# Kernel optimization log

Hardware: AMD Instinct MI355X
Metric: run time of the kernel (lower is better)

The kernel has to match this reference:

```python
import jax, jax.numpy as jnp
import numpy as np
from jax import lax

B, NM, P, F, E, H, K = 32, 131072, 256, 3, 64, 4, 3
DH = E // H


def layer_norm(x, gamma, beta, eps=1e-5):
    mu = x.mean(-1, keepdims=True)
    var = ((x - mu) ** 2).mean(-1, keepdims=True)
    return (x - mu) * lax.rsqrt(var + eps) * gamma + beta


def knn_interp(x, pos_x, pos_y, k=K):
    """x: [B, Nx, F] features at pos_x [Nx, 2]; interpolate to pos_y [Ny, 2].
    Positions are shared across the batch (they are tiled in the torch code),
    so KNN indices/weights are computed once. Matches torch knn + inverse-
    squared-distance weighted scatter (uniform per-batch counts => gather form).
    """
    d2 = jnp.sum((pos_y[:, None, :] - pos_x[None, :, :]) ** 2, axis=-1)  # [Ny, Nx]
    neg_d2, idx = lax.top_k(-d2, k)                                      # [Ny, k]
    w = 1.0 / jnp.clip(-neg_d2, 1e-16)                                   # [Ny, k]
    w = lax.stop_gradient(w)  # torch computes weights under no_grad
    gathered = x[:, idx, :]                                              # [B, Ny, k, F]
    num = jnp.sum(gathered * w[None, :, :, None], axis=2)                # [B, Ny, F]
    den = jnp.sum(w, axis=1)[None, :, None]                              # [1, Ny, 1]
    return num / den


def setup_inputs() -> dict:
    key = jax.random.key(0)
    ks = jax.random.split(key, 8)
    return {
        "node_attr": jax.random.normal(ks[0], (B * NM, F), jnp.float32),
        "position_mesh": jax.random.uniform(ks[1], (NM, 2), jnp.float32),
        "position_pivotal": jax.random.uniform(ks[2], (P, 2), jnp.float32),
        "ln_gamma": jnp.ones((F,), jnp.float32),
        "ln_beta": jnp.zeros((F,), jnp.float32),
        "Wf": jax.random.normal(ks[3], (E, F), jnp.float32) * (2.0 / E) ** 0.5,
        "bf": jnp.zeros((E,), jnp.float32),
        "Wp": jax.random.normal(ks[4], (E, 2), jnp.float32) * (2.0 / E) ** 0.5,
        "bp": jnp.zeros((E,), jnp.float32),
        "in_proj_w": jax.random.normal(ks[5], (3 * E, E), jnp.float32) * (1.0 / E) ** 0.5,
        "in_proj_b": jnp.zeros((3 * E,), jnp.float32),
        "batch_size": B,
    }


def reference(node_attr, position_mesh, position_pivotal, ln_gamma, ln_beta,
              Wf, bf, Wp, bp, in_proj_w, in_proj_b, batch_size):
    x = node_attr.reshape(batch_size, -1, F)                 # [B, NM, F]
    # PivotalNorm after encoder (encoder/decoder MeshGraphNet omitted: undefined dep)
    x = layer_norm(x, ln_gamma, ln_beta)
    # ---- downsample: mesh -> pivotal via inverse-distance KNN interpolation ----
    y = knn_interp(x, position_mesh, position_pivotal)       # [B, P, F]
    # attention-based pooling over pivotal nodes
    q = (jnp.einsum('bpf,ef->bpe', y, Wf) + bf
         + (position_pivotal @ Wp.T + bp)[None])             # [B, P, E]
    Wq, Wk = in_proj_w[:E], in_proj_w[E:2 * E]
    bq, bk = in_proj_b[:E], in_proj_b[E:2 * E]
    Q = (q @ Wq.T + bq).reshape(batch_size, P, H, DH)
    Kt = (q @ Wk.T + bk).reshape(batch_size, P, H, DH)
    scores = jnp.einsum('bqhd,bkhd->bhqk', Q, Kt) / np.float32(np.sqrt(DH))
    attn = jax.nn.softmax(scores, axis=-1)                   # [B, H, P, P]
    attn_w = attn.mean(axis=1)                               # avg heads, [B, P, P]
    y = jnp.einsum('bqk,bkf->bqf', attn_w, y)                # [B, P, F]
    # ---- interpolate: pivotal -> mesh ----
    out = knn_interp(y, position_pivotal, position_mesh)     # [B, NM, F]
    return out.reshape(-1, F)
```

## Files before the change

### kernel.cpp

```cpp
#include <hip/hip_runtime.h>
#include <math.h>

#define NM 131072
#define PP 256
#define BB 32

#define CHUNKS 512
#define CHUNK_SZ 256

#define INF_F 3.0e38f

__device__ __forceinline__ void ins3(float d, int i,
    float& d0, float& d1, float& d2, int& i0, int& i1, int& i2) {
  bool l0 = d < d0, l1 = d < d1, l2 = d < d2;
  d2 = l1 ? d1 : (l2 ? d : d2);
  i2 = l1 ? i1 : (l2 ? i : i2);
  d1 = l0 ? d0 : (l1 ? d : d1);
  i1 = l0 ? i0 : (l1 ? i : i1);
  d0 = l0 ? d : d0;
  i0 = l0 ? i : i0;
}

__device__ __forceinline__ float dist2(float ax, float ay, float bx, float by) {
  float dx = ax - bx, dy = ay - by;
  return __fadd_rn(__fmul_rn(dx, dx), __fmul_rn(dy, dy));
}

__global__ void knnA_partial(const float* __restrict__ mesh, const float* __restrict__ piv,
                             float* __restrict__ candd, int* __restrict__ candi) {
  const int p = threadIdx.x;
  const int c = blockIdx.x;
  const float px = piv[2 * p], py = piv[2 * p + 1];
  float d0 = INF_F, d1 = INF_F, d2 = INF_F;
  int i0 = 0, i1 = 0, i2 = 0;
  const int base = c * CHUNK_SZ;
#pragma unroll 4
  for (int i = 0; i < CHUNK_SZ; ++i) {
    float mx = mesh[2 * (base + i)];
    float my = mesh[2 * (base + i) + 1];
    ins3(dist2(px, py, mx, my), base + i, d0, d1, d2, i0, i1, i2);
  }
  int o = (c * PP + p) * 3;
  candd[o] = d0; candd[o + 1] = d1; candd[o + 2] = d2;
  candi[o] = i0; candi[o + 1] = i1; candi[o + 2] = i2;
}

__global__ void knnA_merge(const float* __restrict__ candd, const int* __restrict__ candi,
                           float* __restrict__ wA, int* __restrict__ idxA) {
  const int p = blockIdx.x;
  const int t = threadIdx.x;
  __shared__ float sd[PP * 3];
  __shared__ int si[PP * 3];
  __shared__ float sd2[32 * 3];
  __shared__ int si2[32 * 3];

  float d0 = INF_F, d1 = INF_F, d2 = INF_F;
  int i0 = 0, i1 = 0, i2 = 0;
  for (int cc = 0; cc < 2; ++cc) {
    int o = ((2 * t + cc) * PP + p) * 3;
    for (int k = 0; k < 3; ++k) ins3(candd[o + k], candi[o + k], d0, d1, d2, i0, i1, i2);
  }
  sd[t * 3] = d0; sd[t * 3 + 1] = d1; sd[t * 3 + 2] = d2;
  si[t * 3] = i0; si[t * 3 + 1] = i1; si[t * 3 + 2] = i2;
  __syncthreads();
  if (t < 32) {
    d0 = d1 = d2 = INF_F; i0 = i1 = i2 = 0;
    for (int j = t * 8; j < t * 8 + 8; ++j)
      for (int k = 0; k < 3; ++k) ins3(sd[j * 3 + k], si[j * 3 + k], d0, d1, d2, i0, i1, i2);
    sd2[t * 3] = d0; sd2[t * 3 + 1] = d1; sd2[t * 3 + 2] = d2;
    si2[t * 3] = i0; si2[t * 3 + 1] = i1; si2[t * 3 + 2] = i2;
  }
  __syncthreads();
  if (t == 0) {
    d0 = d1 = d2 = INF_F; i0 = i1 = i2 = 0;
    for (int j = 0; j < 32; ++j)
      for (int k = 0; k < 3; ++k) ins3(sd2[j * 3 + k], si2[j * 3 + k], d0, d1, d2, i0, i1, i2);
    wA[p * 3 + 0] = 1.0f / fmaxf(d0, 1e-16f); idxA[p * 3 + 0] = i0;
    wA[p * 3 + 1] = 1.0f / fmaxf(d1, 1e-16f); idxA[p * 3 + 1] = i1;
    wA[p * 3 + 2] = 1.0f / fmaxf(d2, 1e-16f); idxA[p * 3 + 2] = i2;
  }
}

__global__ void gather_ln(const float* __restrict__ node, const float* __restrict__ wA,
                          const int* __restrict__ idxA, const float* __restrict__ gamma,
                          const float* __restrict__ beta, float* __restrict__ y) {
  const int b = blockIdx.x >> 2;
  const int p = ((blockIdx.x & 3) << 6) + threadIdx.x;
  const float g0 = gamma[0], g1 = gamma[1], g2 = gamma[2];
  const float be0 = beta[0], be1 = beta[1], be2 = beta[2];
  float num0 = 0.f, num1 = 0.f, num2 = 0.f, den = 0.f;
#pragma unroll
  for (int k = 0; k < 3; ++k) {
    int idx = idxA[p * 3 + k];
    float w = wA[p * 3 + k];
    const float* r = node + ((size_t)b * NM + idx) * 3;
    float a0 = r[0], a1 = r[1], a2 = r[2];
    float mu = (a0 + a1 + a2) * (1.0f / 3.0f);
    float e0 = a0 - mu, e1 = a1 - mu, e2 = a2 - mu;
    float var = (e0 * e0 + e1 * e1 + e2 * e2) * (1.0f / 3.0f);
    float sc = 1.0f / sqrtf(var + 1e-5f);
    float v0 = e0 * sc * g0 + be0, v1 = e1 * sc * g1 + be1, v2 = e2 * sc * g2 + be2;
    num0 += v0 * w; num1 += v1 * w; num2 += v2 * w; den += w;
  }
  int o = (b * PP + p) * 3;
  y[o] = num0 / den; y[o + 1] = num1 / den; y[o + 2] = num2 / den;
}

__global__ void qqk_kernel(const float* __restrict__ y, const float* __restrict__ piv,
                           const float* __restrict__ Wf, const float* __restrict__ bf,
                           const float* __restrict__ Wp, const float* __restrict__ bp,
                           const float* __restrict__ ipw, const float* __restrict__ ipb,
                           float* __restrict__ Qh, float* __restrict__ Kh) {
  const int b = blockIdx.x >> 5;
  const int ptile = (blockIdx.x & 31) * 8;
  const int t = threadIdx.x;
  const int e = t & 63;
  const int half = t >> 6;
  __shared__ float qs[8][64];

  {
    float wf0 = Wf[e * 3], wf1 = Wf[e * 3 + 1], wf2 = Wf[e * 3 + 2];
    float wp0 = Wp[e * 2], wp1 = Wp[e * 2 + 1];
    float cst = bf[e] + bp[e];
    for (int r = half; r < 8; r += 2) {
      int p = ptile + r;
      const float* yr = y + (b * PP + p) * 3;
      float pe = piv[2 * p] * wp0 + piv[2 * p + 1] * wp1;
      qs[r][e] = yr[0] * wf0 + yr[1] * wf1 + yr[2] * wf2 + cst + pe;
    }
  }
  __syncthreads();

  const int row = half * 64 + e;
  float wreg[64];
  const float4* W4 = (const float4*)(ipw + row * 64);
#pragma unroll
  for (int j = 0; j < 16; ++j) {
    float4 v = W4[j];
    wreg[4 * j] = v.x; wreg[4 * j + 1] = v.y; wreg[4 * j + 2] = v.z; wreg[4 * j + 3] = v.w;
  }
  float bias = ipb[row];
  float* dst = half ? Kh : Qh;
  const int h = e >> 4, d = e & 15;
  for (int r = 0; r < 8; ++r) {
    float acc = bias;
#pragma unroll
    for (int j = 0; j < 64; ++j) acc += qs[r][j] * wreg[j];
    int p = ptile + r;
    dst[(((b * 4 + h) * PP) + p) * 16 + d] = acc;
  }
}

__global__ void attn_kernel(const float* __restrict__ Qh, const float* __restrict__ Kh,
                            const float* __restrict__ y, float* __restrict__ y2) {
  const int b = blockIdx.x >> 3;
  const int h = (blockIdx.x >> 1) & 3;
  const int qh = blockIdx.x & 1;
  const int t = threadIdx.x;
  const int q = qh * 128 + t;

  __shared__ float Ks[PP * 16];
  __shared__ float ys[PP * 3];

  {
    const float4* src = (const float4*)(Kh + (size_t)(b * 4 + h) * PP * 16);
    float4* dst = (float4*)Ks;
#pragma unroll
    for (int j = 0; j < 8; ++j) dst[j * 128 + t] = src[j * 128 + t];
    const float* ysrc = y + b * PP * 3;
#pragma unroll
    for (int j = 0; j < 6; ++j) ys[j * 128 + t] = ysrc[j * 128 + t];
  }
  __syncthreads();

  const float4* q4 = (const float4*)(Qh + ((size_t)((b * 4 + h) * PP) + q) * 16);
  float4 qa = q4[0], qb = q4[1], qc = q4[2], qd = q4[3];

  float m = -INF_F, l = 0.f, a0 = 0.f, a1 = 0.f, a2 = 0.f;
#pragma unroll 4
  for (int k = 0; k < PP; ++k) {
    const float4* kr = (const float4*)(Ks + k * 16);
    float4 k0 = kr[0], k1 = kr[1], k2 = kr[2], k3 = kr[3];
    float dot = qa.x * k0.x + qa.y * k0.y + qa.z * k0.z + qa.w * k0.w
              + qb.x * k1.x + qb.y * k1.y + qb.z * k1.z + qb.w * k1.w
              + qc.x * k2.x + qc.y * k2.y + qc.z * k2.z + qc.w * k2.w
              + qd.x * k3.x + qd.y * k3.y + qd.z * k3.z + qd.w * k3.w;
    float s = dot * 0.25f;
    float mn = fmaxf(m, s);
    float p = __expf(s - mn);
    float sc = __expf(m - mn);
    float y0 = ys[k * 3], y1 = ys[k * 3 + 1], yy2 = ys[k * 3 + 2];
    l = l * sc + p;
    a0 = a0 * sc + p * y0;
    a1 = a1 * sc + p * y1;
    a2 = a2 * sc + p * yy2;
    m = mn;
  }
  float inv = 0.25f / l;
  float* o = y2 + (b * PP + q) * 3;
  atomicAdd(o + 0, a0 * inv);
  atomicAdd(o + 1, a1 * inv);
  atomicAdd(o + 2, a2 * inv);
}

__global__ void knnB_out(const float* __restrict__ mesh, const float* __restrict__ piv,
                         const float* __restrict__ y2, float* __restrict__ out) {
  const int m = blockIdx.x * blockDim.x + threadIdx.x;
  const float mx = mesh[2 * m], my = mesh[2 * m + 1];
  float d0 = INF_F, d1 = INF_F, d2 = INF_F;
  int i0 = 0, i1 = 0, i2 = 0;
#pragma unroll 4
  for (int i = 0; i < PP; ++i) {
    float px = piv[2 * i], py = piv[2 * i + 1];
    ins3(dist2(mx, my, px, py), i, d0, d1, d2, i0, i1, i2);
  }
  float w0 = 1.0f / fmaxf(d0, 1e-16f);
  float w1 = 1.0f / fmaxf(d1, 1e-16f);
  float w2 = 1.0f / fmaxf(d2, 1e-16f);
  float inv = 1.0f / (w0 + w1 + w2);
  int o0 = i0 * 3, o1 = i1 * 3, o2 = i2 * 3;
  for (int b = 0; b < BB; ++b) {
    const float* yb = y2 + b * PP * 3;
    float n0 = w0 * yb[o0] + w1 * yb[o1] + w2 * yb[o2];
    float n1 = w0 * yb[o0 + 1] + w1 * yb[o1 + 1] + w2 * yb[o2 + 1];
    float n2 = w0 * yb[o0 + 2] + w1 * yb[o1 + 2] + w2 * yb[o2 + 2];
    float* op = out + ((size_t)b * NM + m) * 3;
    op[0] = n0 * inv; op[1] = n1 * inv; op[2] = n2 * inv;
  }
}

extern "C" void kernel_launch(void* const* d_in, const int* in_sizes, int n_in,
                              void* d_out, int out_size, void* d_ws, size_t ws_size,
                              hipStream_t stream) {
  const float* node  = (const float*)d_in[0];
  const float* mesh  = (const float*)d_in[1];
  const float* piv   = (const float*)d_in[2];
  const float* gamma = (const float*)d_in[3];
  const float* beta  = (const float*)d_in[4];
  const float* Wf    = (const float*)d_in[5];
  const float* bf    = (const float*)d_in[6];
  const float* Wp    = (const float*)d_in[7];
  const float* bp    = (const float*)d_in[8];
  const float* ipw   = (const float*)d_in[9];
  const float* ipb   = (const float*)d_in[10];
  float* out = (float*)d_out;

  float* candd = (float*)d_ws;
  int*   candi = (int*)(candd + CHUNKS * PP * 3);
  float* wA    = (float*)(candi + CHUNKS * PP * 3);
  int*   idxA  = (int*)(wA + PP * 3);
  float* y     = (float*)(idxA + PP * 3);
  float* Qh    = y + BB * PP * 3;
  float* Kh    = Qh + BB * PP * 64;
  float* y2    = Kh + BB * PP * 64;

  hipMemsetAsync(y2, 0, BB * PP * 3 * sizeof(float), stream);

  knnA_partial<<<CHUNKS, PP, 0, stream>>>(mesh, piv, candd, candi);
  knnA_merge<<<PP, 256, 0, stream>>>(candd, candi, wA, idxA);
  gather_ln<<<BB * 4, 64, 0, stream>>>(node, wA, idxA, gamma, beta, y);
  qqk_kernel<<<BB * 32, 128, 0, stream>>>(y, piv, Wf, bf, Wp, bp, ipw, ipb, Qh, Kh);
  attn_kernel<<<BB * 4 * 2, 128, 0, stream>>>(Qh, Kh, y, y2);
  knnB_out<<<NM / 256, 256, 0, stream>>>(mesh, piv, y2, out);
}
```

Before: 224.0 us.

## Split KNN top-3 scans into four independent chains, transpose candidate layout, nontemporal stores

Both KNN scans (mesh->pivotal partial and pivotal->mesh) now keep four independent top-3 lists over interleaved sub-ranges and merge them at the end. This breaks the serial dependency of the insert chain and exposes more instruction-level parallelism. The partial candidate buffer is transposed to a [p][chunk] layout so each merge thread reads contiguous entries. The output kernel also writes through nontemporal stores to avoid polluting caches, and a few unroll pragmas are added. The cost is more live registers, which may lower occupancy. Tie-breaking order among equal distances may also differ from a single sequential scan.

```diff
diff --git a/kernel.cpp b/kernel.cpp
--- a/kernel.cpp
+++ b/kernel.cpp
@@ -31,16 +31,30 @@
   const int p = threadIdx.x;
   const int c = blockIdx.x;
   const float px = piv[2 * p], py = piv[2 * p + 1];
-  float d0 = INF_F, d1 = INF_F, d2 = INF_F;
-  int i0 = 0, i1 = 0, i2 = 0;
+  float D0[4], D1[4], D2[4];
+  int I0[4], I1[4], I2[4];
+#pragma unroll
+  for (int j = 0; j < 4; ++j) { D0[j] = D1[j] = D2[j] = INF_F; I0[j] = I1[j] = I2[j] = 0; }
   const int base = c * CHUNK_SZ;
-#pragma unroll 4
-  for (int i = 0; i < CHUNK_SZ; ++i) {
-    float mx = mesh[2 * (base + i)];
-    float my = mesh[2 * (base + i) + 1];
-    ins3(dist2(px, py, mx, my), base + i, d0, d1, d2, i0, i1, i2);
-  }
-  int o = (c * PP + p) * 3;
+#pragma unroll 2
+  for (int i = 0; i < CHUNK_SZ / 4; ++i) {
+#pragma unroll
+    for (int j = 0; j < 4; ++j) {
+      int idx = base + j * (CHUNK_SZ / 4) + i;
+      float mx = mesh[2 * idx];
+      float my = mesh[2 * idx + 1];
+      ins3(dist2(px, py, mx, my), idx, D0[j], D1[j], D2[j], I0[j], I1[j], I2[j]);
+    }
+  }
+  float d0 = D0[0], d1 = D1[0], d2 = D2[0];
+  int i0 = I0[0], i1 = I1[0], i2 = I2[0];
+#pragma unroll
+  for (int j = 1; j < 4; ++j) {
+    ins3(D0[j], I0[j], d0, d1, d2, i0, i1, i2);
+    ins3(D1[j], I1[j], d0, d1, d2, i0, i1, i2);
+    ins3(D2[j], I2[j], d0, d1, d2, i0, i1, i2);
+  }
+  int o = (p * CHUNKS + c) * 3;
   candd[o] = d0; candd[o + 1] = d1; candd[o + 2] = d2;
   candi[o] = i0; candi[o + 1] = i1; candi[o + 2] = i2;
 }
@@ -56,8 +70,10 @@
 
   float d0 = INF_F, d1 = INF_F, d2 = INF_F;
   int i0 = 0, i1 = 0, i2 = 0;
+#pragma unroll
   for (int cc = 0; cc < 2; ++cc) {
-    int o = ((2 * t + cc) * PP + p) * 3;
+    int o = (p * CHUNKS + 2 * t + cc) * 3;
+#pragma unroll
     for (int k = 0; k < 3; ++k) ins3(candd[o + k], candi[o + k], d0, d1, d2, i0, i1, i2);
   }
   sd[t * 3] = d0; sd[t * 3 + 1] = d1; sd[t * 3 + 2] = d2;
@@ -142,6 +158,7 @@
   float bias = ipb[row];
   float* dst = half ? Kh : Qh;
   const int h = e >> 4, d = e & 15;
+#pragma unroll 2
   for (int r = 0; r < 8; ++r) {
     float acc = bias;
 #pragma unroll
@@ -207,25 +224,42 @@
                          const float* __restrict__ y2, float* __restrict__ out) {
   const int m = blockIdx.x * blockDim.x + threadIdx.x;
   const float mx = mesh[2 * m], my = mesh[2 * m + 1];
-  float d0 = INF_F, d1 = INF_F, d2 = INF_F;
-  int i0 = 0, i1 = 0, i2 = 0;
-#pragma unroll 4
-  for (int i = 0; i < PP; ++i) {
-    float px = piv[2 * i], py = piv[2 * i + 1];
-    ins3(dist2(mx, my, px, py), i, d0, d1, d2, i0, i1, i2);
+  float D0[4], D1[4], D2[4];
+  int I0[4], I1[4], I2[4];
+#pragma unroll
+  for (int j = 0; j < 4; ++j) { D0[j] = D1[j] = D2[j] = INF_F; I0[j] = I1[j] = I2[j] = 0; }
+#pragma unroll 2
+  for (int i = 0; i < PP / 4; ++i) {
+#pragma unroll
+    for (int j = 0; j < 4; ++j) {
+      int idx = j * (PP / 4) + i;
+      float px = piv[2 * idx], py = piv[2 * idx + 1];
+      ins3(dist2(mx, my, px, py), idx, D0[j], D1[j], D2[j], I0[j], I1[j], I2[j]);
+    }
+  }
+  float d0 = D0[0], d1 = D1[0], d2 = D2[0];
+  int i0 = I0[0], i1 = I1[0], i2 = I2[0];
+#pragma unroll
+  for (int j = 1; j < 4; ++j) {
+    ins3(D0[j], I0[j], d0, d1, d2, i0, i1, i2);
+    ins3(D1[j], I1[j], d0, d1, d2, i0, i1, i2);
+    ins3(D2[j], I2[j], d0, d1, d2, i0, i1, i2);
   }
   float w0 = 1.0f / fmaxf(d0, 1e-16f);
   float w1 = 1.0f / fmaxf(d1, 1e-16f);
   float w2 = 1.0f / fmaxf(d2, 1e-16f);
   float inv = 1.0f / (w0 + w1 + w2);
   int o0 = i0 * 3, o1 = i1 * 3, o2 = i2 * 3;
+#pragma unroll 4
   for (int b = 0; b < BB; ++b) {
     const float* yb = y2 + b * PP * 3;
-    float n0 = w0 * yb[o0] + w1 * yb[o1] + w2 * yb[o2];
-    float n1 = w0 * yb[o0 + 1] + w1 * yb[o1 + 1] + w2 * yb[o2 + 1];
-    float n2 = w0 * yb[o0 + 2] + w1 * yb[o1 + 2] + w2 * yb[o2 + 2];
+    float n0 = (w0 * yb[o0] + w1 * yb[o1] + w2 * yb[o2]) * inv;
+    float n1 = (w0 * yb[o0 + 1] + w1 * yb[o1 + 1] + w2 * yb[o2 + 1]) * inv;
+    float n2 = (w0 * yb[o0 + 2] + w1 * yb[o1 + 2] + w2 * yb[o2 + 2]) * inv;
     float* op = out + ((size_t)b * NM + m) * 3;
-    op[0] = n0 * inv; op[1] = n1 * inv; op[2] = n2 * inv;
+    __builtin_nontemporal_store(n0, op + 0);
+    __builtin_nontemporal_store(n1, op + 1);
+    __builtin_nontemporal_store(n2, op + 2);
   }
 }
 
```

Measured after the change: 274.8 us. +22.7%, slower.

## Split KNN scans across sub-threads with shared-memory merge in both KNN kernels

Applied to the files above, without the earlier changes.

knnA_partial now runs 1024 threads per chunk, with four sub-threads per pivot each scanning 64 mesh points. Their top-3 lists are merged through padded shared memory, and candidates are written pivot-major so the merge kernel reads them contiguously. knnB_out likewise splits the 256-pivot scan across four sub-threads per mesh point and divides the 32-batch output loop among them, using float3 loads and stores. This adds parallelism and shortens each thread's serial chain, at the cost of shared-memory traffic, a barrier, and possibly misaligned float3 accesses. qqk_kernel also gets launch bounds.

```diff
diff --git a/kernel.cpp b/kernel.cpp
--- a/kernel.cpp
+++ b/kernel.cpp
@@ -9,6 +9,7 @@
 #define CHUNK_SZ 256
 
 #define INF_F 3.0e38f
+#define LDW 13
 
 __device__ __forceinline__ void ins3(float d, int i,
     float& d0, float& d1, float& d2, int& i0, int& i1, int& i2) {
@@ -26,23 +27,43 @@
   return __fadd_rn(__fmul_rn(dx, dx), __fmul_rn(dy, dy));
 }
 
-__global__ void knnA_partial(const float* __restrict__ mesh, const float* __restrict__ piv,
-                             float* __restrict__ candd, int* __restrict__ candi) {
-  const int p = threadIdx.x;
+__global__ __launch_bounds__(1024)
+void knnA_partial(const float* __restrict__ mesh, const float* __restrict__ piv,
+                  float* __restrict__ candd, int* __restrict__ candi) {
   const int c = blockIdx.x;
-  const float px = piv[2 * p], py = piv[2 * p + 1];
+  const int tid = threadIdx.x;
+  const int p = tid & 255;
+  const int sub = tid >> 8;
+  __shared__ float sdf[256 * LDW];
+  __shared__ int   sif[256 * LDW];
+
+  const float2 pv = ((const float2*)piv)[p];
   float d0 = INF_F, d1 = INF_F, d2 = INF_F;
   int i0 = 0, i1 = 0, i2 = 0;
-  const int base = c * CHUNK_SZ;
+  const int base = c * CHUNK_SZ + sub * 64;
 #pragma unroll 4
-  for (int i = 0; i < CHUNK_SZ; ++i) {
+  for (int i = 0; i < 64; ++i) {
     float mx = mesh[2 * (base + i)];
     float my = mesh[2 * (base + i) + 1];
-    ins3(dist2(px, py, mx, my), base + i, d0, d1, d2, i0, i1, i2);
-  }
-  int o = (c * PP + p) * 3;
-  candd[o] = d0; candd[o + 1] = d1; candd[o + 2] = d2;
-  candi[o] = i0; candi[o + 1] = i1; candi[o + 2] = i2;
+    ins3(dist2(pv.x, pv.y, mx, my), base + i, d0, d1, d2, i0, i1, i2);
+  }
+  sdf[p * LDW + sub * 3 + 0] = d0; sif[p * LDW + sub * 3 + 0] = i0;
+  sdf[p * LDW + sub * 3 + 1] = d1; sif[p * LDW + sub * 3 + 1] = i1;
+  sdf[p * LDW + sub * 3 + 2] = d2; sif[p * LDW + sub * 3 + 2] = i2;
+  __syncthreads();
+
+  if (tid < 256) {
+    float e0 = sdf[tid * LDW + 0], e1 = sdf[tid * LDW + 1], e2 = sdf[tid * LDW + 2];
+    int j0 = sif[tid * LDW + 0], j1 = sif[tid * LDW + 1], j2 = sif[tid * LDW + 2];
+#pragma unroll
+    for (int s = 1; s < 4; ++s)
+#pragma unroll
+      for (int k = 0; k < 3; ++k)
+        ins3(sdf[tid * LDW + s * 3 + k], sif[tid * LDW + s * 3 + k], e0, e1, e2, j0, j1, j2);
+    int o = (tid * CHUNKS + c) * 3;
+    candd[o] = e0; candd[o + 1] = e1; candd[o + 2] = e2;
+    candi[o] = j0; candi[o + 1] = j1; candi[o + 2] = j2;
+  }
 }
 
 __global__ void knnA_merge(const float* __restrict__ candd, const int* __restrict__ candi,
@@ -56,8 +77,10 @@
 
   float d0 = INF_F, d1 = INF_F, d2 = INF_F;
   int i0 = 0, i1 = 0, i2 = 0;
+#pragma unroll
   for (int cc = 0; cc < 2; ++cc) {
-    int o = ((2 * t + cc) * PP + p) * 3;
+    int o = (p * CHUNKS + 2 * t + cc) * 3;
+#pragma unroll
     for (int k = 0; k < 3; ++k) ins3(candd[o + k], candi[o + k], d0, d1, d2, i0, i1, i2);
   }
   sd[t * 3] = d0; sd[t * 3 + 1] = d1; sd[t * 3 + 2] = d2;
@@ -106,11 +129,12 @@
   y[o] = num0 / den; y[o + 1] = num1 / den; y[o + 2] = num2 / den;
 }
 
-__global__ void qqk_kernel(const float* __restrict__ y, const float* __restrict__ piv,
-                           const float* __restrict__ Wf, const float* __restrict__ bf,
-                           const float* __restrict__ Wp, const float* __restrict__ bp,
-                           const float* __restrict__ ipw, const float* __restrict__ ipb,
-                           float* __restrict__ Qh, float* __restrict__ Kh) {
+__global__ __launch_bounds__(128, 2)
+void qqk_kernel(const float* __restrict__ y, const float* __restrict__ piv,
+                const float* __restrict__ Wf, const float* __restrict__ bf,
+                const float* __restrict__ Wp, const float* __restrict__ bp,
+                const float* __restrict__ ipw, const float* __restrict__ ipb,
+                float* __restrict__ Qh, float* __restrict__ Kh) {
   const int b = blockIdx.x >> 5;
   const int ptile = (blockIdx.x & 31) * 8;
   const int t = threadIdx.x;
@@ -203,29 +227,57 @@
   atomicAdd(o + 2, a2 * inv);
 }
 
-__global__ void knnB_out(const float* __restrict__ mesh, const float* __restrict__ piv,
-                         const float* __restrict__ y2, float* __restrict__ out) {
-  const int m = blockIdx.x * blockDim.x + threadIdx.x;
-  const float mx = mesh[2 * m], my = mesh[2 * m + 1];
+__global__ __launch_bounds__(256)
+void knnB_out(const float* __restrict__ mesh, const float* __restrict__ piv,
+              const float* __restrict__ y2, float* __restrict__ out) {
+  const int tid = threadIdx.x;
+  const int ml = tid & 63;
+  const int sub = tid >> 6;
+  const int m = blockIdx.x * 64 + ml;
+  __shared__ float sdf[64 * LDW];
+  __shared__ int   sif[64 * LDW];
+
+  const float2 mv = ((const float2*)mesh)[m];
   float d0 = INF_F, d1 = INF_F, d2 = INF_F;
   int i0 = 0, i1 = 0, i2 = 0;
+  const int base = sub * 64;
 #pragma unroll 4
-  for (int i = 0; i < PP; ++i) {
-    float px = piv[2 * i], py = piv[2 * i + 1];
-    ins3(dist2(mx, my, px, py), i, d0, d1, d2, i0, i1, i2);
-  }
-  float w0 = 1.0f / fmaxf(d0, 1e-16f);
-  float w1 = 1.0f / fmaxf(d1, 1e-16f);
-  float w2 = 1.0f / fmaxf(d2, 1e-16f);
+  for (int i = 0; i < 64; ++i) {
+    int idx = base + i;
+    float px = piv[2 * idx], py = piv[2 * idx + 1];
+    ins3(dist2(mv.x, mv.y, px, py), idx, d0, d1, d2, i0, i1, i2);
+  }
+  sdf[ml * LDW + sub * 3 + 0] = d0; sif[ml * LDW + sub * 3 + 0] = i0;
+  sdf[ml * LDW + sub * 3 + 1] = d1; sif[ml * LDW + sub * 3 + 1] = i1;
+  sdf[ml * LDW + sub * 3 + 2] = d2; sif[ml * LDW + sub * 3 + 2] = i2;
+  __syncthreads();
+
+  float e0 = sdf[ml * LDW + 0], e1 = sdf[ml * LDW + 1], e2 = sdf[ml * LDW + 2];
+  int j0 = sif[ml * LDW + 0], j1 = sif[ml * LDW + 1], j2 = sif[ml * LDW + 2];
+#pragma unroll
+  for (int s = 1; s < 4; ++s)
+#pragma unroll
+    for (int k = 0; k < 3; ++k)
+      ins3(sdf[ml * LDW + s * 3 + k], sif[ml * LDW + s * 3 + k], e0, e1, e2, j0, j1, j2);
+
+  float w0 = 1.0f / fmaxf(e0, 1e-16f);
+  float w1 = 1.0f / fmaxf(e1, 1e-16f);
+  float w2 = 1.0f / fmaxf(e2, 1e-16f);
   float inv = 1.0f / (w0 + w1 + w2);
-  int o0 = i0 * 3, o1 = i1 * 3, o2 = i2 * 3;
-  for (int b = 0; b < BB; ++b) {
+  const int o0 = j0 * 3, o1 = j1 * 3, o2 = j2 * 3;
+
+#pragma unroll 2
+  for (int bi = 0; bi < 8; ++bi) {
+    const int b = sub * 8 + bi;
     const float* yb = y2 + b * PP * 3;
-    float n0 = w0 * yb[o0] + w1 * yb[o1] + w2 * yb[o2];
-    float n1 = w0 * yb[o0 + 1] + w1 * yb[o1 + 1] + w2 * yb[o2 + 1];
-    float n2 = w0 * yb[o0 + 2] + w1 * yb[o1 + 2] + w2 * yb[o2 + 2];
-    float* op = out + ((size_t)b * NM + m) * 3;
-    op[0] = n0 * inv; op[1] = n1 * inv; op[2] = n2 * inv;
+    float3 r0 = *(const float3*)(yb + o0);
+    float3 r1 = *(const float3*)(yb + o1);
+    float3 r2 = *(const float3*)(yb + o2);
+    float3 res;
+    res.x = (w0 * r0.x + w1 * r1.x + w2 * r2.x) * inv;
+    res.y = (w0 * r0.y + w1 * r1.y + w2 * r2.y) * inv;
+    res.z = (w0 * r0.z + w1 * r1.z + w2 * r2.z) * inv;
+    *(float3*)(out + ((size_t)b * NM + m) * 3) = res;
   }
 }
 
@@ -256,10 +308,10 @@
 
   hipMemsetAsync(y2, 0, BB * PP * 3 * sizeof(float), stream);
 
-  knnA_partial<<<CHUNKS, PP, 0, stream>>>(mesh, piv, candd, candi);
+  knnA_partial<<<CHUNKS, 1024, 0, stream>>>(mesh, piv, candd, candi);
   knnA_merge<<<PP, 256, 0, stream>>>(candd, candi, wA, idxA);
   gather_ln<<<BB * 4, 64, 0, stream>>>(node, wA, idxA, gamma, beta, y);
   qqk_kernel<<<BB * 32, 128, 0, stream>>>(y, piv, Wf, bf, Wp, bp, ipw, ipb, Qh, Kh);
   attn_kernel<<<BB * 4 * 2, 128, 0, stream>>>(Qh, Kh, y, y2);
-  knnB_out<<<NM / 256, 256, 0, stream>>>(mesh, piv, y2, out);
-}
+  knnB_out<<<NM / 64, 256, 0, stream>>>(mesh, piv, y2, out);
+}
```

After: 212.5 us. -5.2%, faster.
